# Performance work log

Measured on AMD Instinct MI355X. Metric: run time of the kernel, lower is better.

The kernel has to match this reference:

```python
import jax, jax.numpy as jnp
import numpy as np

NUM_EXPERTS = 64
TOP_K = 8
NORM_TOPK_PROB = True


def setup_inputs() -> dict:
    key = jax.random.key(0)
    k1, k2 = jax.random.split(key)
    hidden_states = jax.random.normal(k1, (8192, 4096), dtype=jnp.float32)
    gate_w = jax.random.normal(k2, (NUM_EXPERTS, 4096), dtype=jnp.float32) * (1.0 / np.sqrt(4096))
    return {"hidden_states": hidden_states, "gate_w": gate_w}


def reference(hidden_states, gate_w):
    # router_logits: (T, E) = hidden @ gate_w.T
    router_logits = jnp.einsum('th,eh->te', hidden_states, gate_w)
    # softmax in float32 (matches F.softmax(..., dtype=torch.float32))
    router_probs = jax.nn.softmax(router_logits.astype(jnp.float32), axis=-1)
    # top-k selection (descending, like torch.topk)
    expert_weights, expert_indices = jax.lax.top_k(router_probs, TOP_K)
    if NORM_TOPK_PROB:
        expert_weights = expert_weights / jnp.sum(expert_weights, axis=-1, keepdims=True)
    expert_weights = expert_weights.astype(hidden_states.dtype)
    # load-balancing loss: N_e * sum_i f_i * p_i
    num_tokens = router_probs.shape[0]
    one_hot = jax.nn.one_hot(expert_indices, NUM_EXPERTS, dtype=jnp.float32)  # (T, K, E)
    tokens_per_expert = one_hot.sum(axis=(0, 1))                              # (E,)
    f = tokens_per_expert / (num_tokens * TOP_K)
    p = router_probs.mean(axis=0)
    aux_loss = NUM_EXPERTS * jnp.sum(f * p)
    return (expert_weights, expert_indices, aux_loss)
```

## Files before the change

kernel.cpp:

```cpp
#include <hip/hip_runtime.h>
#include <math.h>

#define HDIM 4096
#define NEXP 64
#define NTOK 8192
#define KSPLIT 16
#define KSLICE (HDIM / KSPLIT)
#define BM 128
#define CHUNK 32
#define NCHUNK (KSLICE / CHUNK)
#define PSTRIDE 2048
#define CSTRIDE 6144
#define AUXF 1024
#define BSF 393216
#define SLICEOFF (AUXF + BSF)
#define TPW 2

typedef short short8 __attribute__((ext_vector_type(8)));
typedef float f32x4 __attribute__((ext_vector_type(4)));
typedef const __attribute__((address_space(1))) unsigned int* gas_t;
typedef __attribute__((address_space(3))) unsigned int* las_t;

__device__ __forceinline__ void split2x3(float x0, float x1, int& h, int& md, int& lo) {
  unsigned u0 = __float_as_uint(x0), u1 = __float_as_uint(x1);
  unsigned h0 = u0 & 0xFFFF0000u, h1 = u1 & 0xFFFF0000u;
  float r0 = x0 - __uint_as_float(h0);
  float r1 = x1 - __uint_as_float(h1);
  unsigned m0 = __float_as_uint(r0) & 0xFFFF0000u;
  unsigned m1 = __float_as_uint(r1) & 0xFFFF0000u;
  float s0 = r0 - __uint_as_float(m0);
  float s1 = r1 - __uint_as_float(m1);
  h  = (int)((h0 >> 16) | h1);
  md = (int)((m0 >> 16) | m1);
  lo = (int)((__float_as_uint(s0) >> 16) | (__float_as_uint(s1) & 0xFFFF0000u));
}

__device__ __forceinline__ short8 pack_s8(int a, int b, int c, int d) {
  union { int i[4]; short8 s; } u;
  u.i[0] = a; u.i[1] = b; u.i[2] = c; u.i[3] = d;
  return u.s;
}

__global__ void bsplit_k(const float* __restrict__ W, short* __restrict__ Bs) {
  const int e = blockIdx.x;
  const int tid = threadIdx.x;
#pragma unroll
  for (int it = 0; it < 2; ++it) {
    const int k0 = tid * 16 + it * 8;
    const float4 v0 = *(const float4*)&W[(size_t)e * HDIM + k0];
    const float4 v1 = *(const float4*)&W[(size_t)e * HDIM + k0 + 4];
    const float f[8] = {v0.x, v0.y, v0.z, v0.w, v1.x, v1.y, v1.z, v1.w};
    int h[4], md[4], lo[4];
#pragma unroll
    for (int j = 0; j < 4; ++j) split2x3(f[2 * j], f[2 * j + 1], h[j], md[j], lo[j]);
    const int c = k0 >> 5, kk = k0 & 31;
    short* p = Bs + (size_t)c * CSTRIDE + (size_t)e * 32 + kk;
    *(int4*)(p)               = make_int4(h[0], h[1], h[2], h[3]);
    *(int4*)(p + PSTRIDE)     = make_int4(md[0], md[1], md[2], md[3]);
    *(int4*)(p + 2 * PSTRIDE) = make_int4(lo[0], lo[1], lo[2], lo[3]);
  }
}

__global__ __launch_bounds__(256, 4) void gemm_k(const float* __restrict__ A,
                                                 const short* __restrict__ Bs,
                                                 float* __restrict__ Lp,
                                                 int atomic_mode) {
  __shared__ __align__(16) float As[2][BM * CHUNK];
  const int tid = threadIdx.x;
  const int m_base = blockIdx.x * BM;
  const int k_base = blockIdx.y * KSLICE;
  float* Lout = Lp + (atomic_mode ? (size_t)0 : (size_t)blockIdx.y * NTOK * NEXP);

  const int lane = tid & 63;
  const int wave = tid >> 6;
  const int l15 = lane & 15;
  const int quad = lane >> 4;
  const int wm = wave * 32;

  const int rowp = wave * 32 + (lane >> 3);
  const int cblk = (lane & 7) ^ (lane >> 3);
  const float* gA0 = A + (size_t)(m_base + rowp) * HDIM + k_base + cblk * 4;

  auto stageA = [&](int i, int buf) {
#pragma unroll
    for (int j = 0; j < 4; ++j) {
      const float* src = gA0 + (size_t)(j * 8) * HDIM + i * CHUNK;
      __builtin_amdgcn_global_load_lds((gas_t)(const void*)src,
                                       (las_t)(void*)&As[buf][(wave * 4 + j) * 256],
                                       16, 0, 0);
    }
  };

  const short* bbase = Bs + (size_t)(k_base >> 5) * CSTRIDE + (size_t)l15 * 32 + quad * 8;
  short8 breg[12];
  auto loadB = [&](int i) {
    const short* bp = bbase + (size_t)i * CSTRIDE;
#pragma unroll
    for (int nt = 0; nt < 4; ++nt)
#pragma unroll
      for (int p = 0; p < 3; ++p)
        breg[nt * 3 + p] = *(const short8*)(bp + nt * 512 + p * PSTRIDE);
  };

  f32x4 acc[2][4];
#pragma unroll
  for (int mt = 0; mt < 2; ++mt)
#pragma unroll
    for (int nt = 0; nt < 4; ++nt) acc[mt][nt] = (f32x4){0.f, 0.f, 0.f, 0.f};

  stageA(0, 0);
  __syncthreads();

  for (int i = 0; i < NCHUNK; ++i) {
    const int buf = i & 1;
    loadB(i);
    if (i + 1 < NCHUNK) stageA(i + 1, buf ^ 1);

#pragma unroll
    for (int mt = 0; mt < 2; ++mt) {
      const int r = wm + mt * 16 + l15;
      const int rb = r * CHUNK;
      const int sw = r & 7;
      const float4 a0 = *(const float4*)&As[buf][rb + ((2 * quad) ^ sw) * 4];
      const float4 a1 = *(const float4*)&As[buf][rb + ((2 * quad + 1) ^ sw) * 4];
      const float f[8] = {a0.x, a0.y, a0.z, a0.w, a1.x, a1.y, a1.z, a1.w};
      int h[4], md[4], lo[4];
#pragma unroll
      for (int j = 0; j < 4; ++j) split2x3(f[2 * j], f[2 * j + 1], h[j], md[j], lo[j]);
      const short8 fh = pack_s8(h[0], h[1], h[2], h[3]);
      const short8 fm = pack_s8(md[0], md[1], md[2], md[3]);
      const short8 fl = pack_s8(lo[0], lo[1], lo[2], lo[3]);
#pragma unroll
      for (int nt = 0; nt < 4; ++nt) {
        const short8 bh = breg[nt * 3 + 0];
        const short8 bm = breg[nt * 3 + 1];
        const short8 bl = breg[nt * 3 + 2];
        f32x4 c = acc[mt][nt];
        c = __builtin_amdgcn_mfma_f32_16x16x32_bf16(fh, bh, c, 0, 0, 0);
        c = __builtin_amdgcn_mfma_f32_16x16x32_bf16(fh, bm, c, 0, 0, 0);
        c = __builtin_amdgcn_mfma_f32_16x16x32_bf16(fm, bh, c, 0, 0, 0);
        c = __builtin_amdgcn_mfma_f32_16x16x32_bf16(fh, bl, c, 0, 0, 0);
        c = __builtin_amdgcn_mfma_f32_16x16x32_bf16(fl, bh, c, 0, 0, 0);
        c = __builtin_amdgcn_mfma_f32_16x16x32_bf16(fm, bm, c, 0, 0, 0);
        acc[mt][nt] = c;
      }
    }
    __syncthreads();
  }

#pragma unroll
  for (int mt = 0; mt < 2; ++mt)
#pragma unroll
    for (int nt = 0; nt < 4; ++nt)
#pragma unroll
      for (int r = 0; r < 4; ++r) {
        const int m = m_base + wm + mt * 16 + quad * 4 + r;
        const int n = nt * 16 + l15;
        if (atomic_mode) atomicAdd(&Lout[(size_t)m * NEXP + n], acc[mt][nt][r]);
        else Lout[(size_t)m * NEXP + n] = acc[mt][nt][r];
      }
}

__global__ __launch_bounds__(256) void topk_k(const float* __restrict__ Lp, int nsl,
                                              float* __restrict__ out,
                                              float* __restrict__ auxbuf) {
  __shared__ float sl[4][64];
  __shared__ float s_aux[128];
  const int tid = threadIdx.x;
  const int wave = tid >> 6, lane = tid & 63;
  if (tid < 128) s_aux[tid] = 0.f;
  __syncthreads();

  for (int it = 0; it < TPW; ++it) {
    const int t = (blockIdx.x * 4 + wave) * TPW + it;
    float x = 0.f;
    if (nsl == KSPLIT) {
#pragma unroll
      for (int s = 0; s < KSPLIT; ++s)
        x += Lp[(size_t)s * (NTOK * NEXP) + (size_t)t * NEXP + lane];
    } else {
      for (int s = 0; s < nsl; ++s)
        x += Lp[(size_t)s * (NTOK * NEXP) + (size_t)t * NEXP + lane];
    }
    sl[wave][lane] = x;

    float mx = x;
#pragma unroll
    for (int off = 32; off >= 1; off >>= 1)
      mx = fmaxf(mx, __shfl_xor(mx, off, 64));
    const float e = __expf(x - mx);
    float ssum = e;
#pragma unroll
    for (int off = 32; off >= 1; off >>= 1) ssum += __shfl_xor(ssum, off, 64);
    const float prob = e / ssum;

    __syncthreads();

    int cnt = 0;
#pragma unroll
    for (int c = 0; c < 4; ++c) {
      const float4 v0 = *(const float4*)&sl[wave][c * 16 + 0];
      const float4 v1 = *(const float4*)&sl[wave][c * 16 + 4];
      const float4 v2 = *(const float4*)&sl[wave][c * 16 + 8];
      const float4 v3 = *(const float4*)&sl[wave][c * 16 + 12];
      const float xv[16] = {v0.x, v0.y, v0.z, v0.w, v1.x, v1.y, v1.z, v1.w,
                            v2.x, v2.y, v2.z, v2.w, v3.x, v3.y, v3.z, v3.w};
#pragma unroll
      for (int j = 0; j < 16; ++j) {
        const int jj = c * 16 + j;
        cnt += (xv[j] > x) || (xv[j] == x && jj < lane);
      }
    }

    float tp = (cnt < 8) ? prob : 0.f;
    float tsum = tp;
#pragma unroll
    for (int off = 32; off >= 1; off >>= 1) tsum += __shfl_xor(tsum, off, 64);

    const int dst = cnt << 2;
    const float pv = __uint_as_float(
        (unsigned)__builtin_amdgcn_ds_permute(dst, (int)__float_as_uint(prob)));
    const int pi = __builtin_amdgcn_ds_permute(dst, lane);
    if (lane < 8) {
      out[(size_t)t * 8 + lane] = pv / tsum;
      out[(size_t)NTOK * 8 + (size_t)t * 8 + lane] = (float)pi;
    }
    atomicAdd(&s_aux[lane], prob);
    if (cnt < 8) atomicAdd(&s_aux[64 + lane], 1.f);
  }
  __syncthreads();
  if (tid < 128) atomicAdd(&auxbuf[(blockIdx.x & 7) * 128 + tid], s_aux[tid]);
}

__global__ void aux_k(const float* __restrict__ auxbuf, float* __restrict__ out) {
  const int e = threadIdx.x;
  float p = 0.f, f = 0.f;
#pragma unroll
  for (int c = 0; c < 8; ++c) {
    p += auxbuf[c * 128 + e];
    f += auxbuf[c * 128 + 64 + e];
  }
  p *= (1.f / (float)NTOK);
  f *= (1.f / ((float)NTOK * 8.f));
  float v = f * p;
#pragma unroll
  for (int off = 32; off >= 1; off >>= 1) v += __shfl_xor(v, off, 64);
  if (e == 0) out[2 * NTOK * 8] = 64.f * v;
}

extern "C" void kernel_launch(void* const* d_in, const int* in_sizes, int n_in,
                              void* d_out, int out_size, void* d_ws, size_t ws_size,
                              hipStream_t stream) {
  const float* hidden = (const float*)d_in[0];
  const float* gate = (const float*)d_in[1];
  float* out = (float*)d_out;
  float* ws = (float*)d_ws;
  float* auxbuf = ws;
  short* Bs = (short*)(ws + AUXF);
  float* slices = ws + SLICEOFF;

  const size_t need = (size_t)SLICEOFF * 4 + (size_t)KSPLIT * NTOK * NEXP * 4;
  const int atomic_mode = (ws_size < need) ? 1 : 0;
  const int nsl = atomic_mode ? 1 : KSPLIT;

  if (atomic_mode)
    hipMemsetAsync(d_ws, 0, (size_t)SLICEOFF * 4 + (size_t)NTOK * NEXP * 4, stream);
  else
    hipMemsetAsync(d_ws, 0, (size_t)AUXF * 4, stream);

  bsplit_k<<<NEXP, 256, 0, stream>>>(gate, Bs);
  gemm_k<<<dim3(64, KSPLIT), 256, 0, stream>>>(hidden, Bs, slices, atomic_mode);
  topk_k<<<NTOK / (4 * TPW), 256, 0, stream>>>(slices, nsl, out, auxbuf);
  aux_k<<<1, 64, 0, stream>>>(auxbuf, out);
}
```

Before: 227.9 us.

## Fold memset and aux kernel into neighbors; merge GEMM barriers into one per chunk

The auxiliary buffer and completion counter are now zeroed inside bsplit_k instead of by a separate memset. The aux-loss reduction is done by the last topk block, found through an atomic counter, which removes the aux_k launch. In the GEMM loop, the two __syncthreads per chunk become a single s_waitcnt vmcnt(12) plus s_barrier placed after the B loads, so the B register loads can stay in flight across the barrier. The hand-written waitcnt relies on a specific count of outstanding loads, so correctness depends on the compiler emitting exactly that instruction order.

```diff
diff --git a/kernel.cpp b/kernel.cpp
--- a/kernel.cpp
+++ b/kernel.cpp
@@ -11,10 +11,11 @@
 #define NCHUNK (KSLICE / CHUNK)
 #define PSTRIDE 2048
 #define CSTRIDE 6144
-#define AUXF 1024
+#define AUXF 1152
 #define BSF 393216
 #define SLICEOFF (AUXF + BSF)
 #define TPW 2
+#define TOPK_BLOCKS (NTOK / (4 * TPW))
 
 typedef short short8 __attribute__((ext_vector_type(8)));
 typedef float f32x4 __attribute__((ext_vector_type(4)));
@@ -41,9 +42,14 @@
   return u.s;
 }
 
-__global__ void bsplit_k(const float* __restrict__ W, short* __restrict__ Bs) {
+__global__ void bsplit_k(const float* __restrict__ W, short* __restrict__ Bs,
+                         float* __restrict__ wsbase) {
   const int e = blockIdx.x;
   const int tid = threadIdx.x;
+  if (e == 0) {
+#pragma unroll
+    for (int t = tid; t < AUXF; t += 256) wsbase[t] = 0.f;
+  }
 #pragma unroll
   for (int it = 0; it < 2; ++it) {
     const int k0 = tid * 16 + it * 8;
@@ -109,11 +115,13 @@
     for (int nt = 0; nt < 4; ++nt) acc[mt][nt] = (f32x4){0.f, 0.f, 0.f, 0.f};
 
   stageA(0, 0);
-  __syncthreads();
 
   for (int i = 0; i < NCHUNK; ++i) {
     const int buf = i & 1;
     loadB(i);
+    asm volatile("s_waitcnt vmcnt(12)" ::: "memory");
+    __builtin_amdgcn_s_barrier();
+    asm volatile("" ::: "memory");
     if (i + 1 < NCHUNK) stageA(i + 1, buf ^ 1);
 
 #pragma unroll
@@ -145,7 +153,6 @@
         acc[mt][nt] = c;
       }
     }
-    __syncthreads();
   }
 
 #pragma unroll
@@ -163,9 +170,11 @@
 
 __global__ __launch_bounds__(256) void topk_k(const float* __restrict__ Lp, int nsl,
                                               float* __restrict__ out,
-                                              float* __restrict__ auxbuf) {
+                                              float* __restrict__ auxbuf,
+                                              unsigned* __restrict__ counter) {
   __shared__ float sl[4][64];
   __shared__ float s_aux[128];
+  __shared__ int slast;
   const int tid = threadIdx.x;
   const int wave = tid >> 6, lane = tid & 63;
   if (tid < 128) s_aux[tid] = 0.f;
@@ -230,22 +239,31 @@
   }
   __syncthreads();
   if (tid < 128) atomicAdd(&auxbuf[(blockIdx.x & 7) * 128 + tid], s_aux[tid]);
-}
-
-__global__ void aux_k(const float* __restrict__ auxbuf, float* __restrict__ out) {
-  const int e = threadIdx.x;
-  float p = 0.f, f = 0.f;
-#pragma unroll
-  for (int c = 0; c < 8; ++c) {
-    p += auxbuf[c * 128 + e];
-    f += auxbuf[c * 128 + 64 + e];
-  }
-  p *= (1.f / (float)NTOK);
-  f *= (1.f / ((float)NTOK * 8.f));
-  float v = f * p;
-#pragma unroll
-  for (int off = 32; off >= 1; off >>= 1) v += __shfl_xor(v, off, 64);
-  if (e == 0) out[2 * NTOK * 8] = 64.f * v;
+
+  __threadfence();
+  __syncthreads();
+  if (tid == 0) {
+    unsigned done = __hip_atomic_fetch_add(counter, 1u, __ATOMIC_ACQ_REL,
+                                           __HIP_MEMORY_SCOPE_AGENT);
+    slast = (done == (unsigned)(gridDim.x - 1)) ? 1 : 0;
+  }
+  __syncthreads();
+  if (slast && tid < 64) {
+    float p = 0.f, f = 0.f;
+#pragma unroll
+    for (int c = 0; c < 8; ++c) {
+      p += __hip_atomic_load(&auxbuf[c * 128 + tid], __ATOMIC_RELAXED,
+                             __HIP_MEMORY_SCOPE_AGENT);
+      f += __hip_atomic_load(&auxbuf[c * 128 + 64 + tid], __ATOMIC_RELAXED,
+                             __HIP_MEMORY_SCOPE_AGENT);
+    }
+    p *= (1.f / (float)NTOK);
+    f *= (1.f / ((float)NTOK * 8.f));
+    float v = f * p;
+#pragma unroll
+    for (int off = 32; off >= 1; off >>= 1) v += __shfl_xor(v, off, 64);
+    if (tid == 0) out[2 * NTOK * 8] = 64.f * v;
+  }
 }
 
 extern "C" void kernel_launch(void* const* d_in, const int* in_sizes, int n_in,
@@ -256,6 +274,7 @@
   float* out = (float*)d_out;
   float* ws = (float*)d_ws;
   float* auxbuf = ws;
+  unsigned* counter = (unsigned*)(ws + 1024);
   short* Bs = (short*)(ws + AUXF);
   float* slices = ws + SLICEOFF;
 
@@ -265,11 +284,8 @@
 
   if (atomic_mode)
     hipMemsetAsync(d_ws, 0, (size_t)SLICEOFF * 4 + (size_t)NTOK * NEXP * 4, stream);
-  else
-    hipMemsetAsync(d_ws, 0, (size_t)AUXF * 4, stream);
-
-  bsplit_k<<<NEXP, 256, 0, stream>>>(gate, Bs);
+
+  bsplit_k<<<NEXP, 256, 0, stream>>>(gate, Bs, ws);
   gemm_k<<<dim3(64, KSPLIT), 256, 0, stream>>>(hidden, Bs, slices, atomic_mode);
-  topk_k<<<NTOK / (4 * TPW), 256, 0, stream>>>(slices, nsl, out, auxbuf);
-  aux_k<<<1, 64, 0, stream>>>(auxbuf, out);
-}
+  topk_k<<<TOPK_BLOCKS, 256, 0, stream>>>(slices, nsl, out, auxbuf, counter);
+}
```

Measured after the change: 292.5 us. 1.28x slower.

## Merge gemm barriers, batch topk token loads, fold memset, widen aux copies

Applied to the files above, without the earlier changes.

Replaces the two barriers per K-chunk in the GEMM with a single barrier after the B loads, issued once the earlier A loads complete via a manual vmcnt wait. The topk kernel now handles both tokens per wave together, issuing all slice loads up front to raise memory-level parallelism, and uses one barrier instead of one per token. The aux buffer memset is folded into bsplit_k, and the number of atomic aux copies grows to cut contention. The manual waitcnt relies on the exact count of outstanding loads, which risks a race if the compiler reorders the code.

```diff
diff --git a/kernel.cpp b/kernel.cpp
--- a/kernel.cpp
+++ b/kernel.cpp
@@ -11,10 +11,12 @@
 #define NCHUNK (KSLICE / CHUNK)
 #define PSTRIDE 2048
 #define CSTRIDE 6144
-#define AUXF 1024
+#define AUXCOPIES 32
+#define AUXF (AUXCOPIES * 128)
 #define BSF 393216
 #define SLICEOFF (AUXF + BSF)
 #define TPW 2
+#define TOPK_BLOCKS (NTOK / (4 * TPW))
 
 typedef short short8 __attribute__((ext_vector_type(8)));
 typedef float f32x4 __attribute__((ext_vector_type(4)));
@@ -41,9 +43,14 @@
   return u.s;
 }
 
-__global__ void bsplit_k(const float* __restrict__ W, short* __restrict__ Bs) {
+__global__ void bsplit_k(const float* __restrict__ W, short* __restrict__ Bs,
+                         float* __restrict__ wsbase) {
   const int e = blockIdx.x;
   const int tid = threadIdx.x;
+  if (e == 0) {
+#pragma unroll
+    for (int t = tid; t < AUXF; t += 256) wsbase[t] = 0.f;
+  }
 #pragma unroll
   for (int it = 0; it < 2; ++it) {
     const int k0 = tid * 16 + it * 8;
@@ -109,11 +116,13 @@
     for (int nt = 0; nt < 4; ++nt) acc[mt][nt] = (f32x4){0.f, 0.f, 0.f, 0.f};
 
   stageA(0, 0);
-  __syncthreads();
 
   for (int i = 0; i < NCHUNK; ++i) {
     const int buf = i & 1;
     loadB(i);
+    asm volatile("s_waitcnt vmcnt(12)" ::: "memory");
+    __builtin_amdgcn_s_barrier();
+    asm volatile("" ::: "memory");
     if (i + 1 < NCHUNK) stageA(i + 1, buf ^ 1);
 
 #pragma unroll
@@ -145,7 +154,6 @@
         acc[mt][nt] = c;
       }
     }
-    __syncthreads();
   }
 
 #pragma unroll
@@ -164,79 +172,106 @@
 __global__ __launch_bounds__(256) void topk_k(const float* __restrict__ Lp, int nsl,
                                               float* __restrict__ out,
                                               float* __restrict__ auxbuf) {
-  __shared__ float sl[4][64];
+  __shared__ float sl[2][4][64];
   __shared__ float s_aux[128];
   const int tid = threadIdx.x;
   const int wave = tid >> 6, lane = tid & 63;
   if (tid < 128) s_aux[tid] = 0.f;
+
+  const int t0 = (blockIdx.x * 4 + wave) * TPW;
+  float x0 = 0.f, x1 = 0.f;
+  if (nsl == KSPLIT) {
+    float v[2][KSPLIT];
+#pragma unroll
+    for (int tok = 0; tok < 2; ++tok)
+#pragma unroll
+      for (int s = 0; s < KSPLIT; ++s)
+        v[tok][s] = Lp[(size_t)s * (NTOK * NEXP) + (size_t)(t0 + tok) * NEXP + lane];
+#pragma unroll
+    for (int s = 0; s < KSPLIT; ++s) { x0 += v[0][s]; x1 += v[1][s]; }
+  } else {
+    for (int s = 0; s < nsl; ++s) {
+      x0 += Lp[(size_t)s * (NTOK * NEXP) + (size_t)t0 * NEXP + lane];
+      x1 += Lp[(size_t)s * (NTOK * NEXP) + (size_t)(t0 + 1) * NEXP + lane];
+    }
+  }
+  sl[0][wave][lane] = x0;
+  sl[1][wave][lane] = x1;
+
+  float m0 = x0, m1 = x1;
+#pragma unroll
+  for (int off = 32; off >= 1; off >>= 1) {
+    m0 = fmaxf(m0, __shfl_xor(m0, off, 64));
+    m1 = fmaxf(m1, __shfl_xor(m1, off, 64));
+  }
+  const float e0 = __expf(x0 - m0), e1 = __expf(x1 - m1);
+  float ss0 = e0, ss1 = e1;
+#pragma unroll
+  for (int off = 32; off >= 1; off >>= 1) {
+    ss0 += __shfl_xor(ss0, off, 64);
+    ss1 += __shfl_xor(ss1, off, 64);
+  }
+  const float p0 = e0 / ss0, p1 = e1 / ss1;
+
   __syncthreads();
 
-  for (int it = 0; it < TPW; ++it) {
-    const int t = (blockIdx.x * 4 + wave) * TPW + it;
-    float x = 0.f;
-    if (nsl == KSPLIT) {
-#pragma unroll
-      for (int s = 0; s < KSPLIT; ++s)
-        x += Lp[(size_t)s * (NTOK * NEXP) + (size_t)t * NEXP + lane];
-    } else {
-      for (int s = 0; s < nsl; ++s)
-        x += Lp[(size_t)s * (NTOK * NEXP) + (size_t)t * NEXP + lane];
-    }
-    sl[wave][lane] = x;
-
-    float mx = x;
-#pragma unroll
-    for (int off = 32; off >= 1; off >>= 1)
-      mx = fmaxf(mx, __shfl_xor(mx, off, 64));
-    const float e = __expf(x - mx);
-    float ssum = e;
-#pragma unroll
-    for (int off = 32; off >= 1; off >>= 1) ssum += __shfl_xor(ssum, off, 64);
-    const float prob = e / ssum;
-
-    __syncthreads();
-
-    int cnt = 0;
-#pragma unroll
-    for (int c = 0; c < 4; ++c) {
-      const float4 v0 = *(const float4*)&sl[wave][c * 16 + 0];
-      const float4 v1 = *(const float4*)&sl[wave][c * 16 + 4];
-      const float4 v2 = *(const float4*)&sl[wave][c * 16 + 8];
-      const float4 v3 = *(const float4*)&sl[wave][c * 16 + 12];
-      const float xv[16] = {v0.x, v0.y, v0.z, v0.w, v1.x, v1.y, v1.z, v1.w,
-                            v2.x, v2.y, v2.z, v2.w, v3.x, v3.y, v3.z, v3.w};
+  int c0 = 0, c1 = 0;
+#pragma unroll
+  for (int c = 0; c < 4; ++c) {
+#pragma unroll
+    for (int tok = 0; tok < 2; ++tok) {
+      const float4 w0 = *(const float4*)&sl[tok][wave][c * 16 + 0];
+      const float4 w1 = *(const float4*)&sl[tok][wave][c * 16 + 4];
+      const float4 w2 = *(const float4*)&sl[tok][wave][c * 16 + 8];
+      const float4 w3 = *(const float4*)&sl[tok][wave][c * 16 + 12];
+      const float xv[16] = {w0.x, w0.y, w0.z, w0.w, w1.x, w1.y, w1.z, w1.w,
+                            w2.x, w2.y, w2.z, w2.w, w3.x, w3.y, w3.z, w3.w};
+      const float xr = tok ? x1 : x0;
+      int cc = 0;
 #pragma unroll
       for (int j = 0; j < 16; ++j) {
         const int jj = c * 16 + j;
-        cnt += (xv[j] > x) || (xv[j] == x && jj < lane);
+        cc += (xv[j] > xr) || (xv[j] == xr && jj < lane);
       }
+      if (tok) c1 += cc; else c0 += cc;
     }
-
-    float tp = (cnt < 8) ? prob : 0.f;
-    float tsum = tp;
-#pragma unroll
-    for (int off = 32; off >= 1; off >>= 1) tsum += __shfl_xor(tsum, off, 64);
-
-    const int dst = cnt << 2;
-    const float pv = __uint_as_float(
-        (unsigned)__builtin_amdgcn_ds_permute(dst, (int)__float_as_uint(prob)));
-    const int pi = __builtin_amdgcn_ds_permute(dst, lane);
-    if (lane < 8) {
-      out[(size_t)t * 8 + lane] = pv / tsum;
-      out[(size_t)NTOK * 8 + (size_t)t * 8 + lane] = (float)pi;
-    }
-    atomicAdd(&s_aux[lane], prob);
-    if (cnt < 8) atomicAdd(&s_aux[64 + lane], 1.f);
-  }
+  }
+
+  float tp0 = (c0 < 8) ? p0 : 0.f;
+  float tp1 = (c1 < 8) ? p1 : 0.f;
+  float ts0 = tp0, ts1 = tp1;
+#pragma unroll
+  for (int off = 32; off >= 1; off >>= 1) {
+    ts0 += __shfl_xor(ts0, off, 64);
+    ts1 += __shfl_xor(ts1, off, 64);
+  }
+
+  const float pv0 = __uint_as_float(
+      (unsigned)__builtin_amdgcn_ds_permute(c0 << 2, (int)__float_as_uint(p0)));
+  const int pi0 = __builtin_amdgcn_ds_permute(c0 << 2, lane);
+  const float pv1 = __uint_as_float(
+      (unsigned)__builtin_amdgcn_ds_permute(c1 << 2, (int)__float_as_uint(p1)));
+  const int pi1 = __builtin_amdgcn_ds_permute(c1 << 2, lane);
+  if (lane < 8) {
+    out[(size_t)t0 * 8 + lane] = pv0 / ts0;
+    out[(size_t)NTOK * 8 + (size_t)t0 * 8 + lane] = (float)pi0;
+    out[(size_t)(t0 + 1) * 8 + lane] = pv1 / ts1;
+    out[(size_t)NTOK * 8 + (size_t)(t0 + 1) * 8 + lane] = (float)pi1;
+  }
+  atomicAdd(&s_aux[lane], p0 + p1);
+  const float cadd = (c0 < 8 ? 1.f : 0.f) + (c1 < 8 ? 1.f : 0.f);
+  atomicAdd(&s_aux[64 + lane], cadd);
+
   __syncthreads();
-  if (tid < 128) atomicAdd(&auxbuf[(blockIdx.x & 7) * 128 + tid], s_aux[tid]);
+  if (tid < 128)
+    atomicAdd(&auxbuf[(blockIdx.x & (AUXCOPIES - 1)) * 128 + tid], s_aux[tid]);
 }
 
 __global__ void aux_k(const float* __restrict__ auxbuf, float* __restrict__ out) {
   const int e = threadIdx.x;
   float p = 0.f, f = 0.f;
 #pragma unroll
-  for (int c = 0; c < 8; ++c) {
+  for (int c = 0; c < AUXCOPIES; ++c) {
     p += auxbuf[c * 128 + e];
     f += auxbuf[c * 128 + 64 + e];
   }
@@ -265,11 +300,9 @@
 
   if (atomic_mode)
     hipMemsetAsync(d_ws, 0, (size_t)SLICEOFF * 4 + (size_t)NTOK * NEXP * 4, stream);
-  else
-    hipMemsetAsync(d_ws, 0, (size_t)AUXF * 4, stream);
-
-  bsplit_k<<<NEXP, 256, 0, stream>>>(gate, Bs);
+
+  bsplit_k<<<NEXP, 256, 0, stream>>>(gate, Bs, ws);
   gemm_k<<<dim3(64, KSPLIT), 256, 0, stream>>>(hidden, Bs, slices, atomic_mode);
-  topk_k<<<NTOK / (4 * TPW), 256, 0, stream>>>(slices, nsl, out, auxbuf);
+  topk_k<<<TOPK_BLOCKS, 256, 0, stream>>>(slices, nsl, out, auxbuf);
   aux_k<<<1, 64, 0, stream>>>(auxbuf, out);
 }
```

New measurement: 221.8 us. 2.7% less time.
